# Optimization experiments

Hardware: AMD Instinct MI355X
Metric: run time of the kernel (lower is better)

The kernel has to match this reference:

```python
import jax, jax.numpy as jnp
import numpy as np

EMBED_DIM = 1024
NUM_HEADS = 16
HEAD_DIM = EMBED_DIM // NUM_HEADS
SCALE = HEAD_DIM ** -0.5


def setup_inputs() -> dict:
    key = jax.random.key(0)
    ks = jax.random.split(key, 9)
    B, S, D = 32, 577, EMBED_DIM
    std = 1.0 / np.sqrt(D)
    inp = {
        "hidden_states": jax.random.normal(ks[0], (B, S, D), dtype=jnp.float32),
        "q_w": jax.random.normal(ks[1], (D, D), dtype=jnp.float32) * std,
        "q_b": jax.random.normal(ks[2], (D,), dtype=jnp.float32) * 0.01,
        "k_w": jax.random.normal(ks[3], (D, D), dtype=jnp.float32) * std,
        "k_b": jax.random.normal(ks[4], (D,), dtype=jnp.float32) * 0.01,
        "v_w": jax.random.normal(ks[5], (D, D), dtype=jnp.float32) * std,
        "v_b": jax.random.normal(ks[6], (D,), dtype=jnp.float32) * 0.01,
        "o_w": jax.random.normal(ks[7], (D, D), dtype=jnp.float32) * std,
        "o_b": jax.random.normal(ks[8], (D,), dtype=jnp.float32) * 0.01,
    }
    return inp


def reference(hidden_states, q_w, q_b, k_w, k_b, v_w, v_b, o_w, o_b):
    B, S, D = hidden_states.shape
    H, Dh = NUM_HEADS, HEAD_DIM

    def proj(w, b):
        # torch Linear: x @ w.T + b ; reshape to [B, H, S, Dh]
        y = jnp.einsum('bsd,ed->bse', hidden_states, w) + b
        return y.reshape(B, S, H, Dh).transpose(0, 2, 1, 3)

    q = proj(q_w, q_b)
    k = proj(k_w, k_b)
    v = proj(v_w, v_b)

    scores = jnp.einsum('bhqd,bhkd->bhqk', q * SCALE, k)  # [B,H,S,S]
    attn = jax.nn.softmax(scores, axis=-1)
    out = jnp.einsum('bhqk,bhkd->bhqd', attn, v)  # [B,H,S,Dh]
    out = out.transpose(0, 2, 1, 3).reshape(B, S, D)
    return jnp.einsum('bsd,ed->bse', out, o_w) + o_b
```

## Files before the change

### kernel.cpp

```cpp
#include <hip/hip_runtime.h>
#include <hip/hip_bf16.h>
#include <stdint.h>

#define B_   32
#define S_   577
#define SP   640
#define D_   1024
#define H_   16
#define DH   64
#define BH_  (B_*H_)
#define M_   (B_*S_)
#define MP2  18688
#define SCALE_ 0.125f
#define LOG2E_ 1.44269504088896f

typedef __bf16 bf16;
typedef __bf16 bf16x8 __attribute__((ext_vector_type(8)));
typedef __bf16 bf16x4 __attribute__((ext_vector_type(4)));
typedef float  f32x4  __attribute__((ext_vector_type(4)));

__device__ __forceinline__ void gload16(const bf16* g, bf16* l) {
    __builtin_amdgcn_global_load_lds((__attribute__((address_space(1))) void*)g,
                                     (__attribute__((address_space(3))) void*)l, 16, 0, 0);
}

__global__ void cast_all(const float* __restrict__ hs, const float* __restrict__ qw,
                         const float* __restrict__ kw, const float* __restrict__ vw,
                         const float* __restrict__ ow,
                         bf16* __restrict__ hsA, bf16* __restrict__ wq, bf16* __restrict__ wk,
                         bf16* __restrict__ wv, bf16* __restrict__ wo) {
    const int N4H = M_ * 256;
    int i = blockIdx.x * blockDim.x + threadIdx.x;
    if (i >= N4H + 4 * 262144) return;
    const float* in; bf16* out; int r;
    if (i < N4H) { in = hs; out = hsA; r = i; }
    else {
        int j = i - N4H, seg = j >> 18; r = j & 262143;
        in  = (seg == 0) ? qw : (seg == 1) ? kw : (seg == 2) ? vw : ow;
        out = (seg == 0) ? wq : (seg == 1) ? wk : (seg == 2) ? wv : wo;
    }
    float4 v = ((const float4*)in)[r];
    bf16x4 o;
    o[0] = (bf16)v.x; o[1] = (bf16)v.y; o[2] = (bf16)v.z; o[3] = (bf16)v.w;
    ((bf16x4*)out)[r] = o;
}

__global__ void zero_vpad(bf16* __restrict__ vT) {
    int i = blockIdx.x * blockDim.x + threadIdx.x;
    if (i >= BH_ * 64) return;
    bf16* row = vT + (size_t)i * SP + S_;
    #pragma unroll
    for (int j = 0; j < SP - S_; ++j) row[j] = (bf16)0.0f;
}

__device__ __forceinline__ void stage256(const bf16* __restrict__ A, const bf16* __restrict__ B,
                                         int m0, int n0, int K, int kt, bf16* SMbuf) {
    const int tid = threadIdx.x;
    const int wave = tid >> 6;
    #pragma unroll
    for (int ld = 0; ld < 8; ++ld) {
        int li  = ld * 512 + tid;
        int row = (li >> 3) & 255;
        int ch  = (li & 7) ^ (row & 7);
        const bf16* g = ((ld < 4) ? (A + (size_t)(m0 + row) * K)
                                  : (B + (size_t)(n0 + row) * K)) + kt * 64 + ch * 8;
        bf16* l = SMbuf + (size_t)(ld * 512 + wave * 64) * 8;
        gload16(g, l);
    }
}

__device__ __forceinline__ void compute256(const bf16* SMbuf, f32x4 acc[8][4],
                                           int wm, int wn, int r16, int c4) {
    #pragma unroll
    for (int kk = 0; kk < 2; ++kk) {
        bf16x8 bq[4];
        #pragma unroll
        for (int j = 0; j < 4; ++j) {
            int row = wn * 64 + j * 16 + r16;
            int c   = (kk * 4 + c4) ^ (row & 7);
            bq[j] = *(const bf16x8*)(SMbuf + 16384 + row * 64 + c * 8);
        }
        #pragma unroll
        for (int i = 0; i < 8; ++i) {
            int row = wm * 128 + i * 16 + r16;
            int c   = (kk * 4 + c4) ^ (row & 7);
            bf16x8 a = *(const bf16x8*)(SMbuf + row * 64 + c * 8);
            #pragma unroll
            for (int j = 0; j < 4; ++j)
                acc[i][j] = __builtin_amdgcn_mfma_f32_16x16x32_bf16(a, bq[j], acc[i][j], 0, 0, 0);
        }
    }
}

__global__ __launch_bounds__(512, 2) void gemm_qkv(const bf16* __restrict__ A, const bf16* __restrict__ Bw,
                                                   const float* __restrict__ qb, const float* __restrict__ kb,
                                                   const float* __restrict__ vb,
                                                   bf16* __restrict__ qk, bf16* __restrict__ vT) {
    __shared__ __align__(16) bf16 SM[2 * 32768];
    const int bx = blockIdx.x;
    const int bm = bx / 12, bn = bx % 12;
    const int m0 = bm * 256, n0 = bn * 256;
    const int tid = threadIdx.x;
    const int lane = tid & 63, wave = tid >> 6;
    const int wm = wave >> 2, wn = wave & 3;
    const int r16 = lane & 15, c4 = lane >> 4;

    f32x4 acc[8][4];
    #pragma unroll
    for (int i = 0; i < 8; ++i)
        #pragma unroll
        for (int j = 0; j < 4; ++j)
            #pragma unroll
            for (int r = 0; r < 4; ++r) acc[i][j][r] = 0.0f;

    stage256(A, Bw, m0, n0, 1024, 0, SM);
    __syncthreads();
    for (int kt = 0; kt < 16; ++kt) {
        if (kt < 15) stage256(A, Bw, m0, n0, 1024, kt + 1, SM + ((kt + 1) & 1) * 32768);
        compute256(SM + (kt & 1) * 32768, acc, wm, wn, r16, c4);
        __syncthreads();
    }

    if (bn < 8) {
        const float* barr = (bn < 4) ? qb : kb;
        const float mul = (bn < 4) ? SCALE_ * LOG2E_ : 1.0f;
        #pragma unroll
        for (int j = 0; j < 4; ++j) {
            int n = n0 + wn * 64 + j * 16 + r16;
            float bias = barr[n & 1023];
            #pragma unroll
            for (int i = 0; i < 8; ++i) {
                #pragma unroll
                for (int r = 0; r < 4; ++r) {
                    int m = m0 + wm * 128 + i * 16 + c4 * 4 + r;
                    if (m < M_) qk[(size_t)m * 2048 + n] = (bf16)((acc[i][j][r] + bias) * mul);
                }
            }
        }
    } else {
        const int bnp = bn - 8;
        bf16* Ts = SM;
        #pragma unroll
        for (int mh = 0; mh < 2; ++mh) {
            if (wm == mh) {
                #pragma unroll
                for (int j = 0; j < 4; ++j) {
                    int nl = wn * 64 + j * 16 + r16;
                    float bias = vb[bnp * 256 + nl];
                    #pragma unroll
                    for (int i = 0; i < 8; ++i) {
                        #pragma unroll
                        for (int r = 0; r < 4; ++r) {
                            int tr = i * 16 + c4 * 4 + r;
                            Ts[tr * 259 + nl] = (bf16)(acc[i][j][r] + bias);
                        }
                    }
                }
            }
            __syncthreads();
            {
                int ml = tid & 127, nh = tid >> 7;
                int gm = m0 + mh * 128 + ml;
                if (gm < M_) {
                    unsigned bb = (unsigned)gm / 577u, s = (unsigned)gm - bb * 577u;
                    bf16* dst = vT + ((size_t)((bb * 16 + bnp * 4 + nh) * 64)) * SP + s;
                    const bf16* src = Ts + ml * 259 + nh * 64;
                    #pragma unroll 8
                    for (int j = 0; j < 64; ++j) dst[(size_t)j * SP] = src[j];
                }
            }
            __syncthreads();
        }
    }
}

__device__ __forceinline__ void stage_out(const bf16* __restrict__ A, const bf16* __restrict__ B,
                                          int m0, int n0, int kt, bf16* SMbuf) {
    const int tid = threadIdx.x;
    const int wave = tid >> 6;
    #pragma unroll
    for (int ld = 0; ld < 2; ++ld) {
        int li  = ld * 512 + tid;
        int row = li >> 3;
        int ch  = (li & 7) ^ (row & 7);
        gload16(A + (size_t)(m0 + row) * 1024 + kt * 64 + ch * 8,
                SMbuf + (size_t)(ld * 512 + wave * 64) * 8);
    }
    #pragma unroll
    for (int ld = 0; ld < 4; ++ld) {
        int li  = ld * 512 + tid;
        int row = li >> 3;
        int ch  = (li & 7) ^ (row & 7);
        gload16(B + (size_t)(n0 + row) * 1024 + kt * 64 + ch * 8,
                SMbuf + 8192 + (size_t)(ld * 512 + wave * 64) * 8);
    }
}

__global__ __launch_bounds__(512, 2) void gemm_out(const bf16* __restrict__ A, const bf16* __restrict__ Bw,
                                                   const float* __restrict__ ob, float* __restrict__ out) {
    __shared__ __align__(16) bf16 SM[2 * 24576];
    const int bx = blockIdx.x;
    const int bm = bx >> 2, bn = bx & 3;
    const int m0 = bm * 128, n0 = bn * 256;
    const int tid = threadIdx.x;
    const int lane = tid & 63, wave = tid >> 6;
    const int wm = wave >> 2, wn = wave & 3;
    const int r16 = lane & 15, c4 = lane >> 4;

    f32x4 acc[4][4];
    #pragma unroll
    for (int i = 0; i < 4; ++i)
        #pragma unroll
        for (int j = 0; j < 4; ++j)
            #pragma unroll
            for (int r = 0; r < 4; ++r) acc[i][j][r] = 0.0f;

    stage_out(A, Bw, m0, n0, 0, SM);
    __syncthreads();
    for (int kt = 0; kt < 16; ++kt) {
        if (kt < 15) stage_out(A, Bw, m0, n0, kt + 1, SM + ((kt + 1) & 1) * 24576);
        const bf16* SMbuf = SM + (kt & 1) * 24576;
        #pragma unroll
        for (int kk = 0; kk < 2; ++kk) {
            bf16x8 bq[4];
            #pragma unroll
            for (int j = 0; j < 4; ++j) {
                int row = wn * 64 + j * 16 + r16;
                int c   = (kk * 4 + c4) ^ (row & 7);
                bq[j] = *(const bf16x8*)(SMbuf + 8192 + row * 64 + c * 8);
            }
            #pragma unroll
            for (int i = 0; i < 4; ++i) {
                int row = wm * 64 + i * 16 + r16;
                int c   = (kk * 4 + c4) ^ (row & 7);
                bf16x8 a = *(const bf16x8*)(SMbuf + row * 64 + c * 8);
                #pragma unroll
                for (int j = 0; j < 4; ++j)
                    acc[i][j] = __builtin_amdgcn_mfma_f32_16x16x32_bf16(a, bq[j], acc[i][j], 0, 0, 0);
            }
        }
        __syncthreads();
    }

    #pragma unroll
    for (int j = 0; j < 4; ++j) {
        int n = n0 + wn * 64 + j * 16 + r16;
        float bias = ob[n];
        #pragma unroll
        for (int i = 0; i < 4; ++i) {
            #pragma unroll
            for (int r = 0; r < 4; ++r) {
                int m = m0 + wm * 64 + i * 16 + c4 * 4 + r;
                if (m < M_) out[(size_t)m * 1024 + n] = acc[i][j][r] + bias;
            }
        }
    }
}

__global__ __launch_bounds__(256) void attn_kernel(const bf16* __restrict__ qk,
                                                   const bf16* __restrict__ vT, bf16* __restrict__ obuf) {
    __shared__ __align__(16) bf16 KV[2][2][4096];
    __shared__ __align__(16) char Pls[4 * 2048];
    const int orig = blockIdx.x;
    const int xcd = orig & 7;
    const int t   = orig >> 3;
    const int qt  = t % 5, bhg = t / 5;
    const int bh  = bhg * 8 + xcd;
    const int b   = bh >> 4, h = bh & 15;
    const int tid = threadIdx.x;
    const int lane = tid & 63, wave = tid >> 6;
    const int r16 = lane & 15, c4 = lane >> 4;
    const int q0  = qt * 128 + wave * 32;
    const int swz = (r16 & 7) << 4;

    const bf16* qp = qk + (size_t)(b * 577) * 2048 + h * 64;
    const bf16* kp = qp + 1024;
    const bf16* vp = vT + (size_t)bh * 64 * SP;

    bf16x8 aq[2][2];
    #pragma unroll
    for (int qf = 0; qf < 2; ++qf)
        #pragma unroll
        for (int c = 0; c < 2; ++c)
            aq[qf][c] = *(const bf16x8*)(qp + (size_t)(q0 + qf * 16 + r16) * 2048 + c * 32 + c4 * 8);

    float mi[2] = {-3.0e38f, -3.0e38f};
    float li[2] = {0.0f, 0.0f};
    f32x4 accO[2][4];
    #pragma unroll
    for (int qf = 0; qf < 2; ++qf)
        #pragma unroll
        for (int nt = 0; nt < 4; ++nt)
            #pragma unroll
            for (int r = 0; r < 4; ++r) accO[qf][nt][r] = 0.0f;

    char* pbase = Pls + wave * 2048 + r16 * 128;

    auto stageKV = [&](int kt, int buf) {
        #pragma unroll
        for (int half = 0; half < 2; ++half) {
            int li  = half * 256 + tid;
            int row = li >> 3;
            int ch  = (li & 7) ^ (row & 7);
            bf16* lk = &KV[buf][0][(size_t)(half * 256 + wave * 64) * 8];
            bf16* lv = &KV[buf][1][(size_t)(half * 256 + wave * 64) * 8];
            gload16(kp + (size_t)(kt * 64 + row) * 2048 + ch * 8, lk);
            gload16(vp + (size_t)row * SP + kt * 64 + ch * 8, lv);
        }
    };

    stageKV(0, 0);
    __syncthreads();

    for (int kt = 0; kt < 10; ++kt) {
        const int buf = kt & 1;
        if (kt < 9) stageKV(kt + 1, buf ^ 1);

        bf16x8 kf[4][2];
        #pragma unroll
        for (int nt = 0; nt < 4; ++nt)
            #pragma unroll
            for (int c = 0; c < 2; ++c) {
                int row = nt * 16 + r16;
                int cc  = (c * 4 + c4) ^ (row & 7);
                kf[nt][c] = *(const bf16x8*)(&KV[buf][0][row * 64 + cc * 8]);
            }
        f32x4 sc[2][4];
        #pragma unroll
        for (int qf = 0; qf < 2; ++qf)
            #pragma unroll
            for (int nt = 0; nt < 4; ++nt) {
                f32x4 z = {0.0f, 0.0f, 0.0f, 0.0f};
                z = __builtin_amdgcn_mfma_f32_16x16x32_bf16(kf[nt][0], aq[qf][0], z, 0, 0, 0);
                sc[qf][nt] = __builtin_amdgcn_mfma_f32_16x16x32_bf16(kf[nt][1], aq[qf][1], z, 0, 0, 0);
            }

        bf16x8 vf[4][2];
        #pragma unroll
        for (int ntd = 0; ntd < 4; ++ntd)
            #pragma unroll
            for (int kk = 0; kk < 2; ++kk) {
                int row = ntd * 16 + r16;
                int cc  = (kk * 4 + c4) ^ (row & 7);
                vf[ntd][kk] = *(const bf16x8*)(&KV[buf][1][row * 64 + cc * 8]);
            }

        #pragma unroll
        for (int qf = 0; qf < 2; ++qf) {
            if (kt == 9) {
                #pragma unroll
                for (int nt = 0; nt < 4; ++nt)
                    #pragma unroll
                    for (int r = 0; r < 4; ++r)
                        if (576 + nt * 16 + c4 * 4 + r >= S_) sc[qf][nt][r] = -3.0e38f;
            }
            float pmax = sc[qf][0][0];
            #pragma unroll
            for (int nt = 0; nt < 4; ++nt)
                #pragma unroll
                for (int r = 0; r < 4; ++r) pmax = fmaxf(pmax, sc[qf][nt][r]);
            pmax = fmaxf(pmax, __shfl_xor(pmax, 16));
            pmax = fmaxf(pmax, __shfl_xor(pmax, 32));

            const bool vrow = (q0 + qf * 16 + r16) < S_;
            int ok = (!vrow) || (pmax <= mi[qf] + 8.0f);
            if (!__all(ok)) {
                float mnew = fmaxf(mi[qf], pmax);
                float fsc  = __builtin_amdgcn_exp2f(mi[qf] - mnew);
                mi[qf] = mnew;
                li[qf] *= fsc;
                float fs0 = __shfl(fsc, c4 * 4 + 0);
                float fs1 = __shfl(fsc, c4 * 4 + 1);
                float fs2 = __shfl(fsc, c4 * 4 + 2);
                float fs3 = __shfl(fsc, c4 * 4 + 3);
                #pragma unroll
                for (int nt = 0; nt < 4; ++nt) {
                    accO[qf][nt][0] *= fs0; accO[qf][nt][1] *= fs1;
                    accO[qf][nt][2] *= fs2; accO[qf][nt][3] *= fs3;
                }
            }
            float p[4][4];
            float rs = 0.0f;
            #pragma unroll
            for (int nt = 0; nt < 4; ++nt)
                #pragma unroll
                for (int r = 0; r < 4; ++r) {
                    p[nt][r] = __builtin_amdgcn_exp2f(sc[qf][nt][r] - mi[qf]);
                    rs += p[nt][r];
                }
            rs += __shfl_xor(rs, 16);
            rs += __shfl_xor(rs, 32);
            li[qf] += rs;
            #pragma unroll
            for (int nt = 0; nt < 4; ++nt) {
                bf16x4 pk;
                pk[0] = (bf16)p[nt][0]; pk[1] = (bf16)p[nt][1];
                pk[2] = (bf16)p[nt][2]; pk[3] = (bf16)p[nt][3];
                *(bf16x4*)(pbase + ((nt * 32 + c4 * 8) ^ swz)) = pk;
            }

            bf16x8 pf[2];
            #pragma unroll
            for (int kk = 0; kk < 2; ++kk)
                pf[kk] = *(const bf16x8*)(pbase + ((kk * 64 + c4 * 16) ^ swz));
            #pragma unroll
            for (int ntd = 0; ntd < 4; ++ntd)
                #pragma unroll
                for (int kk = 0; kk < 2; ++kk)
                    accO[qf][ntd] = __builtin_amdgcn_mfma_f32_16x16x32_bf16(pf[kk], vf[ntd][kk], accO[qf][ntd], 0, 0, 0);
        }

        __syncthreads();
    }

    #pragma unroll
    for (int qf = 0; qf < 2; ++qf) {
        float inv = 1.0f / li[qf];
        float rl0 = __shfl(inv, c4 * 4 + 0);
        float rl1 = __shfl(inv, c4 * 4 + 1);
        float rl2 = __shfl(inv, c4 * 4 + 2);
        float rl3 = __shfl(inv, c4 * 4 + 3);
        #pragma unroll
        for (int ntd = 0; ntd < 4; ++ntd) {
            #pragma unroll
            for (int r = 0; r < 4; ++r) {
                int s = q0 + qf * 16 + c4 * 4 + r;
                if (s < S_) {
                    float rl = (r == 0) ? rl0 : (r == 1) ? rl1 : (r == 2) ? rl2 : rl3;
                    obuf[((size_t)(b * S_ + s)) * 1024 + h * 64 + ntd * 16 + r16] =
                        (bf16)(accO[qf][ntd][r] * rl);
                }
            }
        }
    }
}

extern "C" void kernel_launch(void* const* d_in, const int* in_sizes, int n_in,
                              void* d_out, int out_size, void* d_ws, size_t ws_size,
                              hipStream_t stream) {
    const float* hs = (const float*)d_in[0];
    const float* qw = (const float*)d_in[1];
    const float* qb = (const float*)d_in[2];
    const float* kw = (const float*)d_in[3];
    const float* kb = (const float*)d_in[4];
    const float* vw = (const float*)d_in[5];
    const float* vb = (const float*)d_in[6];
    const float* ow = (const float*)d_in[7];
    const float* ob = (const float*)d_in[8];

    char* ws = (char*)d_ws;
    size_t off = 0;
    auto alloc = [&](size_t bytes) { void* p = ws + off; off += (bytes + 255) & ~255UL; return p; };
    bf16* hsA  = (bf16*)alloc((size_t)MP2 * 1024 * 2);
    bf16* wqkv = (bf16*)alloc((size_t)3072 * 1024 * 2);
    bf16* wo   = (bf16*)alloc((size_t)1024 * 1024 * 2);
    bf16* qk   = (bf16*)alloc((size_t)MP2 * 2048 * 2);
    bf16* vT   = (bf16*)alloc((size_t)BH_ * 64 * SP * 2);

    zero_vpad<<<(BH_ * 64 + 255) / 256, 256, 0, stream>>>(vT);

    int n4all = M_ * 256 + 4 * 262144;
    cast_all<<<(n4all + 255) / 256, 256, 0, stream>>>(hs, qw, kw, vw, ow,
                                                      hsA, wqkv, wqkv + 1048576, wqkv + 2097152, wo);

    gemm_qkv<<<73 * 12, 512, 0, stream>>>(hsA, wqkv, qb, kb, vb, qk, vT);
    attn_kernel<<<2560, 256, 0, stream>>>(qk, vT, hsA);
    gemm_out<<<145 * 4, 512, 0, stream>>>(hsA, wo, ob, (float*)d_out);
}
```

Before: 361.1 us.

## Enlarge attention query tile to 256 rows with 8 waves, fuse vpad zeroing

```diff
diff --git a/kernel.cpp b/kernel.cpp
--- a/kernel.cpp
+++ b/kernel.cpp
@@ -28,29 +28,30 @@
                          const float* __restrict__ kw, const float* __restrict__ vw,
                          const float* __restrict__ ow,
                          bf16* __restrict__ hsA, bf16* __restrict__ wq, bf16* __restrict__ wk,
-                         bf16* __restrict__ wv, bf16* __restrict__ wo) {
+                         bf16* __restrict__ wv, bf16* __restrict__ wo, bf16* __restrict__ vT) {
     const int N4H = M_ * 256;
+    const int N4W = 4 * 262144;
     int i = blockIdx.x * blockDim.x + threadIdx.x;
-    if (i >= N4H + 4 * 262144) return;
-    const float* in; bf16* out; int r;
-    if (i < N4H) { in = hs; out = hsA; r = i; }
-    else {
-        int j = i - N4H, seg = j >> 18; r = j & 262143;
-        in  = (seg == 0) ? qw : (seg == 1) ? kw : (seg == 2) ? vw : ow;
-        out = (seg == 0) ? wq : (seg == 1) ? wk : (seg == 2) ? wv : wo;
-    }
-    float4 v = ((const float4*)in)[r];
-    bf16x4 o;
-    o[0] = (bf16)v.x; o[1] = (bf16)v.y; o[2] = (bf16)v.z; o[3] = (bf16)v.w;
-    ((bf16x4*)out)[r] = o;
-}
-
-__global__ void zero_vpad(bf16* __restrict__ vT) {
-    int i = blockIdx.x * blockDim.x + threadIdx.x;
-    if (i >= BH_ * 64) return;
-    bf16* row = vT + (size_t)i * SP + S_;
-    #pragma unroll
-    for (int j = 0; j < SP - S_; ++j) row[j] = (bf16)0.0f;
+    if (i < N4H + N4W) {
+        const float* in; bf16* out; int r;
+        if (i < N4H) { in = hs; out = hsA; r = i; }
+        else {
+            int j = i - N4H, seg = j >> 18; r = j & 262143;
+            in  = (seg == 0) ? qw : (seg == 1) ? kw : (seg == 2) ? vw : ow;
+            out = (seg == 0) ? wq : (seg == 1) ? wk : (seg == 2) ? wv : wo;
+        }
+        float4 v = ((const float4*)in)[r];
+        bf16x4 o;
+        o[0] = (bf16)v.x; o[1] = (bf16)v.y; o[2] = (bf16)v.z; o[3] = (bf16)v.w;
+        ((bf16x4*)out)[r] = o;
+    } else {
+        int j = i - (N4H + N4W);
+        if (j < BH_ * 64) {
+            bf16* row = vT + (size_t)j * SP + S_;
+            #pragma unroll
+            for (int k = 0; k < SP - S_; ++k) row[k] = (bf16)0.0f;
+        }
+    }
 }
 
 __device__ __forceinline__ void stage256(const bf16* __restrict__ A, const bf16* __restrict__ B,
@@ -257,26 +258,29 @@
     }
 }
 
-__global__ __launch_bounds__(256) void attn_kernel(const bf16* __restrict__ qk,
+__global__ __launch_bounds__(512) void attn_kernel(const bf16* __restrict__ qk,
                                                    const bf16* __restrict__ vT, bf16* __restrict__ obuf) {
     __shared__ __align__(16) bf16 KV[2][2][4096];
-    __shared__ __align__(16) char Pls[4 * 2048];
+    __shared__ __align__(16) char Pls[8 * 2048];
     const int orig = blockIdx.x;
     const int xcd = orig & 7;
     const int t   = orig >> 3;
-    const int qt  = t % 5, bhg = t / 5;
+    const int qt  = t % 3, bhg = t / 3;
     const int bh  = bhg * 8 + xcd;
     const int b   = bh >> 4, h = bh & 15;
     const int tid = threadIdx.x;
     const int lane = tid & 63, wave = tid >> 6;
     const int r16 = lane & 15, c4 = lane >> 4;
-    const int q0  = qt * 128 + wave * 32;
+    const int q0  = qt * 256 + wave * 32;
     const int swz = (r16 & 7) << 4;
 
     const bf16* qp = qk + (size_t)(b * 577) * 2048 + h * 64;
     const bf16* kp = qp + 1024;
     const bf16* vp = vT + (size_t)bh * 64 * SP;
 
+    const bool live0 = (q0 < S_);
+    const bool live1 = (q0 + 16 < S_);
+
     bf16x8 aq[2][2];
     #pragma unroll
     for (int qf = 0; qf < 2; ++qf)
@@ -297,16 +301,12 @@
     char* pbase = Pls + wave * 2048 + r16 * 128;
 
     auto stageKV = [&](int kt, int buf) {
-        #pragma unroll
-        for (int half = 0; half < 2; ++half) {
-            int li  = half * 256 + tid;
-            int row = li >> 3;
-            int ch  = (li & 7) ^ (row & 7);
-            bf16* lk = &KV[buf][0][(size_t)(half * 256 + wave * 64) * 8];
-            bf16* lv = &KV[buf][1][(size_t)(half * 256 + wave * 64) * 8];
-            gload16(kp + (size_t)(kt * 64 + row) * 2048 + ch * 8, lk);
-            gload16(vp + (size_t)row * SP + kt * 64 + ch * 8, lv);
-        }
+        int row = tid >> 3;
+        int ch  = (tid & 7) ^ (row & 7);
+        gload16(kp + (size_t)(kt * 64 + row) * 2048 + ch * 8,
+                &KV[buf][0][(size_t)(wave * 64) * 8]);
+        gload16(vp + (size_t)row * SP + kt * 64 + ch * 8,
+                &KV[buf][1][(size_t)(wave * 64) * 8]);
     };
 
     stageKV(0, 0);
@@ -316,98 +316,105 @@
         const int buf = kt & 1;
         if (kt < 9) stageKV(kt + 1, buf ^ 1);
 
-        bf16x8 kf[4][2];
-        #pragma unroll
-        for (int nt = 0; nt < 4; ++nt)
-            #pragma unroll
-            for (int c = 0; c < 2; ++c) {
-                int row = nt * 16 + r16;
-                int cc  = (c * 4 + c4) ^ (row & 7);
-                kf[nt][c] = *(const bf16x8*)(&KV[buf][0][row * 64 + cc * 8]);
-            }
-        f32x4 sc[2][4];
-        #pragma unroll
-        for (int qf = 0; qf < 2; ++qf)
-            #pragma unroll
-            for (int nt = 0; nt < 4; ++nt) {
-                f32x4 z = {0.0f, 0.0f, 0.0f, 0.0f};
-                z = __builtin_amdgcn_mfma_f32_16x16x32_bf16(kf[nt][0], aq[qf][0], z, 0, 0, 0);
-                sc[qf][nt] = __builtin_amdgcn_mfma_f32_16x16x32_bf16(kf[nt][1], aq[qf][1], z, 0, 0, 0);
-            }
-
-        bf16x8 vf[4][2];
-        #pragma unroll
-        for (int ntd = 0; ntd < 4; ++ntd)
-            #pragma unroll
-            for (int kk = 0; kk < 2; ++kk) {
-                int row = ntd * 16 + r16;
-                int cc  = (kk * 4 + c4) ^ (row & 7);
-                vf[ntd][kk] = *(const bf16x8*)(&KV[buf][1][row * 64 + cc * 8]);
-            }
-
-        #pragma unroll
-        for (int qf = 0; qf < 2; ++qf) {
-            if (kt == 9) {
+        if (live0) {
+            bf16x8 kf[4][2];
+            #pragma unroll
+            for (int nt = 0; nt < 4; ++nt)
+                #pragma unroll
+                for (int c = 0; c < 2; ++c) {
+                    int row = nt * 16 + r16;
+                    int cc  = (c * 4 + c4) ^ (row & 7);
+                    kf[nt][c] = *(const bf16x8*)(&KV[buf][0][row * 64 + cc * 8]);
+                }
+            f32x4 sc[2][4];
+            __builtin_amdgcn_s_setprio(1);
+            #pragma unroll
+            for (int qf = 0; qf < 2; ++qf)
+                #pragma unroll
+                for (int nt = 0; nt < 4; ++nt) {
+                    f32x4 z = {0.0f, 0.0f, 0.0f, 0.0f};
+                    z = __builtin_amdgcn_mfma_f32_16x16x32_bf16(kf[nt][0], aq[qf][0], z, 0, 0, 0);
+                    sc[qf][nt] = __builtin_amdgcn_mfma_f32_16x16x32_bf16(kf[nt][1], aq[qf][1], z, 0, 0, 0);
+                }
+            __builtin_amdgcn_s_setprio(0);
+
+            bf16x8 vf[4][2];
+            #pragma unroll
+            for (int ntd = 0; ntd < 4; ++ntd)
+                #pragma unroll
+                for (int kk = 0; kk < 2; ++kk) {
+                    int row = ntd * 16 + r16;
+                    int cc  = (kk * 4 + c4) ^ (row & 7);
+                    vf[ntd][kk] = *(const bf16x8*)(&KV[buf][1][row * 64 + cc * 8]);
+                }
+
+            #pragma unroll
+            for (int qf = 0; qf < 2; ++qf) {
+                if (qf == 1 && !live1) continue;
+                if (kt == 9) {
+                    #pragma unroll
+                    for (int nt = 0; nt < 4; ++nt)
+                        #pragma unroll
+                        for (int r = 0; r < 4; ++r)
+                            if (576 + nt * 16 + c4 * 4 + r >= S_) sc[qf][nt][r] = -3.0e38f;
+                }
+                float pmax = sc[qf][0][0];
                 #pragma unroll
                 for (int nt = 0; nt < 4; ++nt)
                     #pragma unroll
-                    for (int r = 0; r < 4; ++r)
-                        if (576 + nt * 16 + c4 * 4 + r >= S_) sc[qf][nt][r] = -3.0e38f;
-            }
-            float pmax = sc[qf][0][0];
-            #pragma unroll
-            for (int nt = 0; nt < 4; ++nt)
-                #pragma unroll
-                for (int r = 0; r < 4; ++r) pmax = fmaxf(pmax, sc[qf][nt][r]);
-            pmax = fmaxf(pmax, __shfl_xor(pmax, 16));
-            pmax = fmaxf(pmax, __shfl_xor(pmax, 32));
-
-            const bool vrow = (q0 + qf * 16 + r16) < S_;
-            int ok = (!vrow) || (pmax <= mi[qf] + 8.0f);
-            if (!__all(ok)) {
-                float mnew = fmaxf(mi[qf], pmax);
-                float fsc  = __builtin_amdgcn_exp2f(mi[qf] - mnew);
-                mi[qf] = mnew;
-                li[qf] *= fsc;
-                float fs0 = __shfl(fsc, c4 * 4 + 0);
-                float fs1 = __shfl(fsc, c4 * 4 + 1);
-                float fs2 = __shfl(fsc, c4 * 4 + 2);
-                float fs3 = __shfl(fsc, c4 * 4 + 3);
+                    for (int r = 0; r < 4; ++r) pmax = fmaxf(pmax, sc[qf][nt][r]);
+                pmax = fmaxf(pmax, __shfl_xor(pmax, 16));
+                pmax = fmaxf(pmax, __shfl_xor(pmax, 32));
+
+                const bool vrow = (q0 + qf * 16 + r16) < S_;
+                int ok = (!vrow) || (pmax <= mi[qf] + 8.0f);
+                if (!__all(ok)) {
+                    float mnew = fmaxf(mi[qf], pmax);
+                    float fsc  = __builtin_amdgcn_exp2f(mi[qf] - mnew);
+                    mi[qf] = mnew;
+                    li[qf] *= fsc;
+                    float fs0 = __shfl(fsc, c4 * 4 + 0);
+                    float fs1 = __shfl(fsc, c4 * 4 + 1);
+                    float fs2 = __shfl(fsc, c4 * 4 + 2);
+                    float fs3 = __shfl(fsc, c4 * 4 + 3);
+                    #pragma unroll
+                    for (int nt = 0; nt < 4; ++nt) {
+                        accO[qf][nt][0] *= fs0; accO[qf][nt][1] *= fs1;
+                        accO[qf][nt][2] *= fs2; accO[qf][nt][3] *= fs3;
+                    }
+                }
+                float p[4][4];
+                float rs = 0.0f;
+                #pragma unroll
+                for (int nt = 0; nt < 4; ++nt)
+                    #pragma unroll
+                    for (int r = 0; r < 4; ++r) {
+                        p[nt][r] = __builtin_amdgcn_exp2f(sc[qf][nt][r] - mi[qf]);
+                        rs += p[nt][r];
+                    }
+                rs += __shfl_xor(rs, 16);
+                rs += __shfl_xor(rs, 32);
+                li[qf] += rs;
                 #pragma unroll
                 for (int nt = 0; nt < 4; ++nt) {
-                    accO[qf][nt][0] *= fs0; accO[qf][nt][1] *= fs1;
-                    accO[qf][nt][2] *= fs2; accO[qf][nt][3] *= fs3;
-                }
-            }
-            float p[4][4];
-            float rs = 0.0f;
-            #pragma unroll
-            for (int nt = 0; nt < 4; ++nt)
-                #pragma unroll
-                for (int r = 0; r < 4; ++r) {
-                    p[nt][r] = __builtin_amdgcn_exp2f(sc[qf][nt][r] - mi[qf]);
-                    rs += p[nt][r];
-                }
-            rs += __shfl_xor(rs, 16);
-            rs += __shfl_xor(rs, 32);
-            li[qf] += rs;
-            #pragma unroll
-            for (int nt = 0; nt < 4; ++nt) {
-                bf16x4 pk;
-                pk[0] = (bf16)p[nt][0]; pk[1] = (bf16)p[nt][1];
-                pk[2] = (bf16)p[nt][2]; pk[3] = (bf16)p[nt][3];
-                *(bf16x4*)(pbase + ((nt * 32 + c4 * 8) ^ swz)) = pk;
-            }
-
-            bf16x8 pf[2];
-            #pragma unroll
-            for (int kk = 0; kk < 2; ++kk)
-                pf[kk] = *(const bf16x8*)(pbase + ((kk * 64 + c4 * 16) ^ swz));
-            #pragma unroll
-            for (int ntd = 0; ntd < 4; ++ntd)
+                    bf16x4 pk;
+                    pk[0] = (bf16)p[nt][0]; pk[1] = (bf16)p[nt][1];
+                    pk[2] = (bf16)p[nt][2]; pk[3] = (bf16)p[nt][3];
+                    *(bf16x4*)(pbase + ((nt * 32 + c4 * 8) ^ swz)) = pk;
+                }
+
+                bf16x8 pf[2];
                 #pragma unroll
                 for (int kk = 0; kk < 2; ++kk)
-                    accO[qf][ntd] = __builtin_amdgcn_mfma_f32_16x16x32_bf16(pf[kk], vf[ntd][kk], accO[qf][ntd], 0, 0, 0);
+                    pf[kk] = *(const bf16x8*)(pbase + ((kk * 64 + c4 * 16) ^ swz));
+                __builtin_amdgcn_s_setprio(1);
+                #pragma unroll
+                for (int ntd = 0; ntd < 4; ++ntd)
+                    #pragma unroll
+                    for (int kk = 0; kk < 2; ++kk)
+                        accO[qf][ntd] = __builtin_amdgcn_mfma_f32_16x16x32_bf16(pf[kk], vf[ntd][kk], accO[qf][ntd], 0, 0, 0);
+                __builtin_amdgcn_s_setprio(0);
+            }
         }
 
         __syncthreads();
@@ -415,6 +422,7 @@
 
     #pragma unroll
     for (int qf = 0; qf < 2; ++qf) {
+        if (q0 + qf * 16 >= S_) continue;
         float inv = 1.0f / li[qf];
         float rl0 = __shfl(inv, c4 * 4 + 0);
         float rl1 = __shfl(inv, c4 * 4 + 1);
@@ -457,13 +465,11 @@
     bf16* qk   = (bf16*)alloc((size_t)MP2 * 2048 * 2);
     bf16* vT   = (bf16*)alloc((size_t)BH_ * 64 * SP * 2);
 
-    zero_vpad<<<(BH_ * 64 + 255) / 256, 256, 0, stream>>>(vT);
-
-    int n4all = M_ * 256 + 4 * 262144;
+    int n4all = M_ * 256 + 4 * 262144 + BH_ * 64;
     cast_all<<<(n4all + 255) / 256, 256, 0, stream>>>(hs, qw, kw, vw, ow,
-                                                      hsA, wqkv, wqkv + 1048576, wqkv + 2097152, wo);
+                                                      hsA, wqkv, wqkv + 1048576, wqkv + 2097152, wo, vT);
 
     gemm_qkv<<<73 * 12, 512, 0, stream>>>(hsA, wqkv, qb, kb, vb, qk, vT);
-    attn_kernel<<<2560, 256, 0, stream>>>(qk, vT, hsA);
+    attn_kernel<<<1536, 512, 0, stream>>>(qk, vT, hsA);
     gemm_out<<<145 * 4, 512, 0, stream>>>(hsA, wo, ob, (float*)d_out);
 }
```

After: 377.5 us. +4.6%, slower.
